# Kernel tuning notes

Measured on AMD Instinct MI355X. Metric: run time of the kernel, lower is better.

Reference implementation:

```python
import jax, jax.numpy as jnp
from jax import lax
import numpy as np

# ---- static configuration (RPN inference path) ----
B = 8
IMG_H, IMG_W = 800, 1216
LEVEL_GRIDS = [(200, 304), (100, 152), (50, 76), (25, 38), (13, 19)]
STRIDES = [4, 8, 16, 32, 64]
SIZES = [32, 64, 128, 256, 512]
RATIOS = np.array([0.5, 1.0, 2.0])
NUM_PER_LEVEL = [h * w * 3 for (h, w) in LEVEL_GRIDS]  # [182400,45600,11400,2850,741]
A_TOTAL = sum(NUM_PER_LEVEL)                            # 242991
PRE_N = 1000   # pre_nms_top_n['testing'], applied per level
POST_N = 1000  # post_nms_top_n['testing']
NMS_THRESH = 0.7
SCORE_THRESH = 0.0
MIN_SIZE = 0.001
BBOX_XFORM_CLIP = float(np.log(1000.0 / 16.0))
LEVEL_OFFSET = 4096.0  # > max image coord, for batched_nms level separation

K_PER_LEVEL = [min(PRE_N, n) for n in NUM_PER_LEVEL]
K_TOTAL = sum(K_PER_LEVEL)  # 4741
LEVELS = jnp.concatenate([jnp.full((k,), i, dtype=jnp.int32)
                          for i, k in enumerate(K_PER_LEVEL)])


def _make_anchors():
    """torchvision-style grid anchors, one scale + 3 aspect ratios per level."""
    all_anchors = []
    for (fh, fw), stride, size in zip(LEVEL_GRIDS, STRIDES, SIZES):
        h_ratios = np.sqrt(RATIOS)
        w_ratios = 1.0 / h_ratios
        ws = w_ratios * size
        hs = h_ratios * size
        base = np.stack([-ws / 2, -hs / 2, ws / 2, hs / 2], axis=1)  # [3,4]
        sx = np.arange(fw, dtype=np.float32) * stride
        sy = np.arange(fh, dtype=np.float32) * stride
        yy, xx = np.meshgrid(sy, sx, indexing='ij')
        shifts = np.stack([xx, yy, xx, yy], axis=-1).reshape(-1, 1, 4)  # [fh*fw,1,4]
        anchors = (shifts + base[None]).reshape(-1, 4)                  # [fh*fw*3,4]
        all_anchors.append(anchors.astype(np.float32))
    return np.concatenate(all_anchors, axis=0)  # [A_TOTAL,4]


def setup_inputs() -> dict:
    key = jax.random.key(0)
    k1, k2 = jax.random.split(key)
    objectness = jax.random.normal(k1, (B, A_TOTAL), dtype=jnp.float32)
    pred_bbox_deltas = jax.random.normal(k2, (B, A_TOTAL, 4), dtype=jnp.float32) * 0.5
    anchors = jnp.asarray(_make_anchors())
    return {"objectness": objectness, "pred_bbox_deltas": pred_bbox_deltas,
            "anchors": anchors}


def _decode(deltas, anchors):
    """BoxCoder.decode with weights (1,1,1,1). deltas [B,A,4], anchors [A,4]."""
    wa = anchors[:, 2] - anchors[:, 0]
    ha = anchors[:, 3] - anchors[:, 1]
    cxa = anchors[:, 0] + 0.5 * wa
    cya = anchors[:, 1] + 0.5 * ha
    dx, dy, dw, dh = deltas[..., 0], deltas[..., 1], deltas[..., 2], deltas[..., 3]
    dw = jnp.minimum(dw, BBOX_XFORM_CLIP)
    dh = jnp.minimum(dh, BBOX_XFORM_CLIP)
    cx = dx * wa + cxa
    cy = dy * ha + cya
    w = jnp.exp(dw) * wa
    h = jnp.exp(dh) * ha
    return jnp.stack([cx - 0.5 * w, cy - 0.5 * h, cx + 0.5 * w, cy + 0.5 * h], axis=-1)


def _per_level_topk(objectness):
    """_get_top_n_idx: per-level top-k with global offsets. Returns [B,K_TOTAL] int32."""
    idxs, offset = [], 0
    for n, k in zip(NUM_PER_LEVEL, K_PER_LEVEL):
        _, ti = lax.top_k(objectness[:, offset:offset + n], k)
        idxs.append(ti + offset)
        offset += n
    return jnp.concatenate(idxs, axis=1)


def _iou(boxes):  # boxes [K,4] -> [K,K]
    area = (boxes[:, 2] - boxes[:, 0]) * (boxes[:, 3] - boxes[:, 1])
    lt = jnp.maximum(boxes[:, None, :2], boxes[None, :, :2])
    rb = jnp.minimum(boxes[:, None, 2:], boxes[None, :, 2:])
    wh = jnp.clip(rb - lt, 0.0)
    inter = wh[..., 0] * wh[..., 1]
    return inter / (area[:, None] + area[None, :] - inter)


def _nms_image(boxes, scores, levels, valid):
    """clip->filter->batched_nms->post_nms_top_n for one image (fixed shapes)."""
    K = boxes.shape[0]
    order = jnp.argsort(-jnp.where(valid, scores, -jnp.inf))
    b = boxes[order]
    s = scores[order]
    v = valid[order]
    lv = levels[order]
    # batched NMS: offset boxes by level so cross-level boxes never overlap
    bb = b + lv.astype(b.dtype)[:, None] * LEVEL_OFFSET
    iou = lax.stop_gradient(_iou(bb))  # keep decisions are non-differentiable
    idxr = jnp.arange(K)

    def body(i, keep):
        sup = (iou[i] > NMS_THRESH) & (idxr > i) & keep[i]
        return keep & ~sup

    keep = lax.fori_loop(0, K, body, v)
    sel = jnp.where(keep, s, -1.0)  # sigmoid scores are > 0
    top_s, top_i = lax.top_k(sel, POST_N)
    kept = top_s > 0.0
    out_b = jnp.where(kept[:, None], b[top_i], 0.0)
    out_s = jnp.where(kept, top_s, 0.0)
    return out_b, out_s


def reference(objectness, pred_bbox_deltas, anchors):
    # box decode for all anchors
    proposals = _decode(pred_bbox_deltas, anchors)          # [B,A,4]
    # per-level topk + gather
    idx = _per_level_topk(objectness)                       # [B,K]
    obj = jnp.take_along_axis(objectness, idx, axis=1)      # [B,K]
    props = jnp.take_along_axis(proposals, idx[..., None], axis=1)  # [B,K,4]
    scores = jax.nn.sigmoid(obj)
    lv = jnp.broadcast_to(LEVELS, idx.shape)
    # clip_boxes_to_image
    x1 = jnp.clip(props[..., 0], 0.0, IMG_W)
    y1 = jnp.clip(props[..., 1], 0.0, IMG_H)
    x2 = jnp.clip(props[..., 2], 0.0, IMG_W)
    y2 = jnp.clip(props[..., 3], 0.0, IMG_H)
    props = jnp.stack([x1, y1, x2, y2], axis=-1)
    # remove_small_boxes + score_thresh
    valid = (x2 - x1 >= MIN_SIZE) & (y2 - y1 >= MIN_SIZE) & (scores >= SCORE_THRESH)
    boxes_out, scores_out = jax.vmap(_nms_image)(props, scores, lv, valid)
    return boxes_out, scores_out  # [B,POST_N,4], [B,POST_N] (zero-padded)
```

## Files before the change

### kernel.cpp

```cpp
#include <hip/hip_runtime.h>
#include <stdint.h>

#pragma clang fp contract(off)

typedef unsigned int u32;
typedef unsigned long long u64;

#define A_TOTAL 242991
#define KTOT    4741

__constant__ int c_LN[5]   = {182400, 45600, 11400, 2850, 741};
__constant__ int c_LOFF[5] = {0, 182400, 228000, 239400, 242250};
__constant__ int c_LK[5]   = {1000, 1000, 1000, 1000, 741};

__constant__ int c_SL[33] = {0,0,0,0,0,0,0,0,0,0,0,0,0,0,0,0,0,0,0,0,0,0,0,
                             1,1,1,1,1,1, 2,2, 3, 4};
__constant__ int c_SS[33] = {0,8192,16384,24576,32768,40960,49152,57344,65536,
                             73728,81920,90112,98304,106496,114688,122880,131072,
                             139264,147456,155648,163840,172032,180224,
                             0,8192,16384,24576,32768,40960, 0,8192, 0, 0};

__constant__ int c_MW[40] = {0,1,2,3, 4,4, 5,5, 6,6, 7,7, 8,8,8, 9,9,9,
                             10,10,10, 11,11,11, 12,12,12,12, 13,13,13,13,
                             14,14,14,14, 15,15,15,15};
__constant__ int c_MR[40] = {0,0,0,0, 0,1, 0,1, 0,1, 0,1, 0,1,2, 0,1,2,
                             0,1,2, 0,1,2, 0,1,2,3, 0,1,2,3,
                             0,1,2,3, 0,1,2,3};

static const size_t OFF_KEEPW    = 0;
static const size_t OFF_HIST     = 0;
static const size_t OFF_SELCNT   = 327680;
static const size_t OFF_CANDCNT  = 327840;
static const size_t OFF_TBIN     = 328000;
static const size_t OFF_CLESS    = 328160;
static const size_t OFF_SELG     = 328320;
static const size_t OFF_CANDG    = 656000;
static const size_t OFF_BOX      = 2270144;
static const size_t OFF_SCORE    = 2876992;
static const size_t OFF_VALID    = 3028704;
static const size_t OFF_MASK     = 3180416;
static const size_t OFF_OUTK     = 8423296;

__device__ __forceinline__ u32 fmap(float f){
  u32 b = __float_as_uint(f);
  return (b & 0x80000000u) ? ~b : (b | 0x80000000u);
}
__device__ __forceinline__ float funmap(u32 m){
  return __uint_as_float((m & 0x80000000u) ? (m & 0x7FFFFFFFu) : ~m);
}

#define ZWS  82000
#define ZOUT 40000
__global__ void __launch_bounds__(256)
k_zero(u32* __restrict__ ws0, u32* __restrict__ outw)
{
  int i = blockIdx.x * 256 + (int)threadIdx.x;
  if (i < ZWS) ws0[i] = 0u;
  else {
    int j = i - ZWS;
    if (j < ZOUT) outw[j] = 0u;
  }
}

__global__ void __launch_bounds__(1024)
k_hist(const float* __restrict__ obj, u32* __restrict__ hist)
{
  int b = blockIdx.x / 33, s = blockIdx.x % 33;
  int l = c_SL[s], start = c_SS[s];
  int cnt = c_LN[l] - start; if (cnt > 8192) cnt = 8192;
  int bl = b * 5 + l;
  __shared__ u32 h[4][2048];
  for (int i = threadIdx.x; i < 8192; i += 1024) ((u32*)h)[i] = 0;
  __syncthreads();
  u32* hw = h[(threadIdx.x >> 6) & 3];
  const float* p = obj + (size_t)b * A_TOTAL + c_LOFF[l] + start;
  int head = (4 - (int)(((size_t)p >> 2) & 3)) & 3;
  if (head > cnt) head = cnt;
  if ((int)threadIdx.x < head) atomicAdd(&hw[(~fmap(p[threadIdx.x])) >> 21], 1u);
  int nvec = (cnt - head) >> 2;
  const float4* pv = (const float4*)(p + head);
  for (int i = threadIdx.x; i < nvec; i += 1024){
    float4 v = pv[i];
    atomicAdd(&hw[(~fmap(v.x)) >> 21], 1u);
    atomicAdd(&hw[(~fmap(v.y)) >> 21], 1u);
    atomicAdd(&hw[(~fmap(v.z)) >> 21], 1u);
    atomicAdd(&hw[(~fmap(v.w)) >> 21], 1u);
  }
  int tail0 = head + (nvec << 2);
  int ntail = cnt - tail0;
  if ((int)threadIdx.x < ntail) atomicAdd(&hw[(~fmap(p[tail0 + threadIdx.x])) >> 21], 1u);
  __syncthreads();
  for (int i = threadIdx.x; i < 2048; i += 1024){
    u32 v = h[0][i] + h[1][i] + h[2][i] + h[3][i];
    if (v) atomicAdd(&hist[bl * 2048 + i], v);
  }
}

__global__ void __launch_bounds__(256)
k_cutoff(u32* __restrict__ hist, u32* __restrict__ tbin, u32* __restrict__ cless)
{
  int bl = blockIdx.x; int l = bl % 5;
  int K = c_LK[l], n = c_LN[l];
  int tid = threadIdx.x;
  __shared__ u32 cum[2048];
  __shared__ u32 part[256];
  __shared__ int s_t;
  u32 vals[8]; u32 sum = 0;
  for (int q = 0; q < 8; ++q){ vals[q] = hist[bl * 2048 + tid * 8 + q]; sum += vals[q]; }
  part[tid] = sum;
  __syncthreads();
  for (int off = 1; off < 256; off <<= 1){
    u32 add = (tid >= off) ? part[tid - off] : 0u;
    __syncthreads();
    part[tid] += add;
    __syncthreads();
  }
  u32 run = (tid > 0) ? part[tid - 1] : 0u;
  for (int q = 0; q < 8; ++q){ run += vals[q]; cum[tid * 8 + q] = run; }
  __syncthreads();
  if (K >= n){ if (tid == 0){ tbin[bl] = 2048u; cless[bl] = (u32)n; } return; }
  if (tid == 0) s_t = 0;
  __syncthreads();
  for (int q = 0; q < 8; ++q){
    int i = tid * 8 + q;
    u32 c = cum[i], cp = (i > 0) ? cum[i - 1] : 0u;
    if (c >= (u32)K && cp < (u32)K) s_t = i;
  }
  __syncthreads();
  if (tid == 0){
    int t = s_t;
    tbin[bl] = (u32)t;
    cless[bl] = (t > 0) ? cum[t - 1] : 0u;
  }
}

#define SELCAP 2048
#define CANDCAP 1024
__global__ void __launch_bounds__(1024)
k_collect(const float* __restrict__ obj, const u32* __restrict__ tbin,
          u32* __restrict__ selcnt, u32* __restrict__ candcnt,
          u64* __restrict__ selg, u64* __restrict__ candg)
{
  int b = blockIdx.x / 33, s = blockIdx.x % 33;
  int l = c_SL[s], start = c_SS[s];
  int cnt = c_LN[l] - start; if (cnt > 8192) cnt = 8192;
  int bl = b * 5 + l;
  u32 t = tbin[bl];
  __shared__ u64 lsel[SELCAP];
  __shared__ u64 lcand[CANDCAP];
  __shared__ u32 lcs, lcc, gbs, gbc;
  if (threadIdx.x == 0){ lcs = 0u; lcc = 0u; }
  __syncthreads();
  const float* p = obj + (size_t)b * A_TOTAL + c_LOFF[l] + start;

  auto push = [&](u32 m, int idx){
    u32 bin = m >> 21;
    u64 key = ((u64)m << 32) | (u32)idx;
    if (bin < t){
      u32 pos = atomicAdd(&lcs, 1u);
      if (pos < SELCAP) lsel[pos] = key;
      else { u32 gp = atomicAdd(&selcnt[bl], 1u); selg[(size_t)bl * 1024 + gp] = key; }
    } else if (bin == t){
      u32 pos = atomicAdd(&lcc, 1u);
      if (pos < CANDCAP) lcand[pos] = key;
      else { u32 gp = atomicAdd(&candcnt[bl], 1u); if (gp < 4096u) candg[(size_t)bl * 4096 + gp] = key; }
    }
  };

  int head = (4 - (int)(((size_t)p >> 2) & 3)) & 3;
  if (head > cnt) head = cnt;
  if ((int)threadIdx.x < head) push(~fmap(p[threadIdx.x]), start + (int)threadIdx.x);
  int nvec = (cnt - head) >> 2;
  const float4* pv = (const float4*)(p + head);
  for (int i = threadIdx.x; i < nvec; i += 1024){
    float4 v = pv[i];
    int e = start + head + (i << 2);
    push(~fmap(v.x), e);
    push(~fmap(v.y), e + 1);
    push(~fmap(v.z), e + 2);
    push(~fmap(v.w), e + 3);
  }
  int tail0 = head + (nvec << 2);
  int ntail = cnt - tail0;
  if ((int)threadIdx.x < ntail) push(~fmap(p[tail0 + threadIdx.x]), start + tail0 + (int)threadIdx.x);
  __syncthreads();
  u32 ns = lcs;  if (ns > SELCAP) ns = SELCAP;
  u32 ncd = lcc; if (ncd > CANDCAP) ncd = CANDCAP;
  if (threadIdx.x == 0){
    gbs = ns  ? atomicAdd(&selcnt[bl],  ns)  : 0u;
    gbc = ncd ? atomicAdd(&candcnt[bl], ncd) : 0u;
  }
  __syncthreads();
  u32 bs = gbs, bc = gbc;
  for (u32 i = threadIdx.x; i < ns; i += 1024)
    selg[(size_t)bl * 1024 + bs + i] = lsel[i];
  for (u32 i = threadIdx.x; i < ncd; i += 1024){
    u32 gp = bc + i;
    if (gp < 4096u) candg[(size_t)bl * 4096 + gp] = lcand[i];
  }
}

__global__ void __launch_bounds__(1024)
k_selectdec(const u32* __restrict__ selcnt, const u32* __restrict__ candcnt,
            const u64* __restrict__ selg, const u64* __restrict__ candg,
            const float* __restrict__ deltas, const float* __restrict__ anchors,
            float* __restrict__ boxes, float* __restrict__ scores, u32* __restrict__ valid)
{
  int bl = blockIdx.x; int b = bl / 5, l = bl % 5;
  int K = c_LK[l];
  int tid = threadIdx.x;
  __shared__ __align__(16) u64 selU[1024];
  __shared__ __align__(16) u64 candU[4098];
  __shared__ u64 keysL[1000];
  u32 ns = selcnt[bl]; if (ns > 1024u) ns = 1024u;
  u32 nc = candcnt[bl]; if (nc > 4096u) nc = 4096u;
  int R = K - (int)ns;
  selU[tid] = (tid < (int)ns) ? selg[(size_t)bl * 1024 + tid] : ~0ULL;
  for (u32 i = tid; i < nc; i += 1024) candU[i] = candg[(size_t)bl * 4096 + i];
  u32 nce = (nc + 1u) & ~1u;
  if (tid == 0 && nce > nc) candU[nc] = ~0ULL;
  __syncthreads();
  if (tid < (int)ns){
    u64 key = selU[tid];
    u32 r = 0;
    #pragma unroll 8
    for (u32 j = 0; j < 1024; j += 2){
      ulonglong2 v = *reinterpret_cast<const ulonglong2*>(&selU[j]);
      r += (v.x < key) + (v.y < key);
    }
    keysL[r] = key;
  }
  if (R > 0){
    for (u32 s = tid; s < nc; s += 1024){
      u64 key = candU[s];
      u32 r = 0;
      #pragma unroll 8
      for (u32 j = 0; j < nce; j += 2){
        ulonglong2 v = *reinterpret_cast<const ulonglong2*>(&candU[j]);
        r += (v.x < key) + (v.y < key);
      }
      if (r < (u32)R) keysL[ns + r] = key;
    }
  }
  __syncthreads();
  if (tid < K){
    u64 key = keysL[tid];
    int g = b * KTOT + l * 1000 + tid;
    u32 idx = (u32)key;
    float o = funmap(~(u32)(key >> 32));
    int ai = c_LOFF[l] + (int)idx;
    const float* a = anchors + (size_t)ai * 4;
    const float* d = deltas + ((size_t)b * A_TOTAL + ai) * 4;
    float a0 = a[0], a1 = a[1], a2 = a[2], a3 = a[3];
    float wa = __fsub_rn(a2, a0), ha = __fsub_rn(a3, a1);
    float cxa = __fadd_rn(a0, __fmul_rn(0.5f, wa));
    float cya = __fadd_rn(a1, __fmul_rn(0.5f, ha));
    float dx = d[0], dy = d[1];
    float dw = fminf(d[2], 4.135166556742356f);
    float dh = fminf(d[3], 4.135166556742356f);
    float cx = __fadd_rn(__fmul_rn(dx, wa), cxa);
    float cy = __fadd_rn(__fmul_rn(dy, ha), cya);
    float w  = __fmul_rn(expf(dw), wa);
    float h  = __fmul_rn(expf(dh), ha);
    float hw = __fmul_rn(0.5f, w), hh = __fmul_rn(0.5f, h);
    float x1 = __fsub_rn(cx, hw), y1 = __fsub_rn(cy, hh);
    float x2 = __fadd_rn(cx, hw), y2 = __fadd_rn(cy, hh);
    x1 = fminf(fmaxf(x1, 0.0f), 1216.0f);
    x2 = fminf(fmaxf(x2, 0.0f), 1216.0f);
    y1 = fminf(fmaxf(y1, 0.0f), 800.0f);
    y2 = fminf(fmaxf(y2, 0.0f), 800.0f);
    float s = __fdiv_rn(1.0f, __fadd_rn(1.0f, expf(-o)));
    int v = (__fsub_rn(x2, x1) >= 0.001f) && (__fsub_rn(y2, y1) >= 0.001f) && (s >= 0.0f);
    float* bo = boxes + (size_t)g * 4;
    bo[0] = x1; bo[1] = y1; bo[2] = x2; bo[3] = y2;
    scores[g] = s;
    valid[g] = (u32)v;
  }
}

__global__ void __launch_bounds__(256)
k_mask(const float* __restrict__ boxes, u64* __restrict__ mask)
{
  int b = blockIdx.x / 184, s = blockIdx.x % 184;
  int l, idx;
  if (s < 160){ l = s / 40; idx = s % 40; }
  else        { l = 4;      idx = s - 160; }
  int w = c_MW[idx], rb = c_MR[idx];
  int N = c_LK[l];
  int koff = l * 1000;
  float offv = (float)(l * 4096);
  __shared__ float sjx1[64], sjy1[64], sjx2[64], sjy2[64], sjar[64];
  int jbase = w * 64;
  if (threadIdx.x < 64){
    int j = jbase + (int)threadIdx.x;
    float x1, y1, x2, y2, ar;
    if (j < N){
      float4 p = ((const float4*)boxes)[(size_t)(b * KTOT + koff + j)];
      x1 = __fadd_rn(p.x, offv); y1 = __fadd_rn(p.y, offv);
      x2 = __fadd_rn(p.z, offv); y2 = __fadd_rn(p.w, offv);
      ar = __fmul_rn(__fsub_rn(x2, x1), __fsub_rn(y2, y1));
    } else {
      x1 = 3e38f; y1 = 3e38f; x2 = -3e38f; y2 = -3e38f; ar = 0.f;
    }
    sjx1[threadIdx.x] = x1; sjy1[threadIdx.x] = y1;
    sjx2[threadIdx.x] = x2; sjy2[threadIdx.x] = y2; sjar[threadIdx.x] = ar;
  }
  __syncthreads();
  int i = rb * 256 + (int)threadIdx.x;
  int rows = (w + 1) * 64; if (rows > N) rows = N;
  if (i >= rows) return;
  float4 p = ((const float4*)boxes)[(size_t)(b * KTOT + koff + i)];
  float bx1 = __fadd_rn(p.x, offv), by1 = __fadd_rn(p.y, offv);
  float bx2 = __fadd_rn(p.z, offv), by2 = __fadd_rn(p.w, offv);
  float bar = __fmul_rn(__fsub_rn(bx2, bx1), __fsub_rn(by2, by1));
  u64 bw = 0;
  #pragma unroll 16
  for (int jj = 0; jj < 64; ++jj){
    int j = jbase + jj;
    float ltx = fmaxf(bx1, sjx1[jj]), lty = fmaxf(by1, sjy1[jj]);
    float rbx = fminf(bx2, sjx2[jj]), rby = fminf(by2, sjy2[jj]);
    float wx = fmaxf(__fsub_rn(rbx, ltx), 0.0f);
    float wy = fmaxf(__fsub_rn(rby, lty), 0.0f);
    float inter = __fmul_rn(wx, wy);
    bool sup = false;
    if (inter > 0.0f && j > i){
      float den = __fsub_rn(__fadd_rn(bar, sjar[jj]), inter);
      sup = __fdiv_rn(inter, den) > 0.7f;
    }
    bw |= ((u64)sup) << jj;
  }
  mask[((size_t)(b * 5 + l) * 16 + w) * 1024 + i] = bw;
}

__global__ void __launch_bounds__(256)
k_nms(const u64* __restrict__ mask, const u32* __restrict__ valid,
      const float* __restrict__ scores, u64* __restrict__ outk,
      u64* __restrict__ keepw)
{
  int bl = blockIdx.x; int b = bl / 5, l = bl % 5;
  int N = c_LK[l], koff = l * 1000;
  int WN = (N + 63) >> 6;
  int tid = threadIdx.x;
  __shared__ u64 s_kw[16];
  __shared__ u64 s_m[7680];
  const u64* mb = mask + (size_t)bl * 16 * 1024;
  int wstage = (WN < 15) ? WN : 15;
  for (int w = 0; w < wstage; ++w){
    int rows = (w + 1) * 64;
    int base = 32 * w * (w + 1);
    for (int r = tid; r < rows; r += 256)
      s_m[base + r] = mb[(size_t)w * 1024 + r];
  }
  __syncthreads();
  if (tid < 64){
    int lane = tid;
    for (int c = 0; c < WN; ++c){
      int i = c * 64 + lane;
      int pred = (i < N) && (valid[(size_t)b * KTOT + koff + i] != 0u);
      u64 bal = __ballot(pred);
      if (lane == 0) s_kw[c] = bal;
    }
    for (int w = 0; w < WN; ++w){
      u64 kwv = s_kw[w];
      u64 supl = 0;
      if (w < 15){
        int base = 32 * w * (w + 1);
        for (int jb = 0; jb < w; ++jb){
          u64 kb = s_kw[jb];
          u64 m = s_m[base + jb * 64 + lane];
          supl |= (((kb >> lane) & 1ULL) ? m : 0ULL);
        }
      } else {
        for (int jb = 0; jb < w; ++jb){
          u64 kb = s_kw[jb];
          u64 m = mb[(size_t)w * 1024 + jb * 64 + lane];
          supl |= (((kb >> lane) & 1ULL) ? m : 0ULL);
        }
      }
      int jr = w * 64 + lane;
      u64 rowl;
      if (w < 15) rowl = s_m[32 * w * (w + 1) + jr];
      else        rowl = (jr < N) ? mb[(size_t)w * 1024 + jr] : 0ULL;
      bool inC = ((kwv >> lane) & 1ULL) != 0ULL;
      u64 rkw = rowl & kwv;
      u64 confl = inC ? rkw : 0ULL;
      u32 a0 = (u32)supl, a1 = (u32)(supl >> 32);
      u32 a2 = (u32)confl, a3 = (u32)(confl >> 32);
      for (int off = 32; off; off >>= 1){
        a0 |= __shfl_xor(a0, off);
        a1 |= __shfl_xor(a1, off);
        a2 |= __shfl_xor(a2, off);
        a3 |= __shfl_xor(a3, off);
      }
      supl = ((u64)a1 << 32) | a0;
      u64 conf = ((u64)a3 << 32) | a2;
      u64 srcb = __ballot(inC && (rkw != 0ULL));
      u64 cur = kwv & ~supl;
      u64 kept = cur;
      if (((srcb & cur) != 0ULL) && ((conf & cur) != 0ULL)){
        u32 rowl_lo = (u32)rowl, rowl_hi = (u32)(rowl >> 32);
        u64 act = cur & (srcb | conf);
        while (act){
          int ib  = __ffsll((unsigned long long)act) - 1;
          int ibs = __builtin_amdgcn_readfirstlane(ib);
          u64 bit = 1ULL << ibs;
          act &= ~bit;
          if (kept & bit){
            u32 rlo = (u32)__builtin_amdgcn_readlane((int)rowl_lo, ibs);
            u32 rhi = (u32)__builtin_amdgcn_readlane((int)rowl_hi, ibs);
            u64 r   = ((u64)rhi << 32) | rlo;
            kept &= ~r;
            act  &= ~r;
          }
        }
      }
      if (lane == 0) s_kw[w] = kept;
    }
  }
  __syncthreads();
  if (tid < 16) keepw[(size_t)bl * 16 + tid] = (tid < WN) ? s_kw[tid] : 0ULL;
  for (int i = tid; i < N; i += 256){
    u64 key = ~0ULL;
    if ((s_kw[i >> 6] >> (i & 63)) & 1ULL){
      float sc = scores[(size_t)b * KTOT + koff + i];
      key = ((u64)(~fmap(sc)) << 32) | (u32)(koff + i);
    }
    outk[(size_t)b * KTOT + koff + i] = key;
  }
}

#define CMPN 1024
__global__ void __launch_bounds__(256)
k_rank(const u64* __restrict__ outk, const u64* __restrict__ keepw,
       const float* __restrict__ boxes, float* __restrict__ out)
{
  int b = blockIdx.x / 19, chunk = blockIdx.x % 19;
  int tid = threadIdx.x;
  __shared__ u64 cmp[5 * CMPN];
  __shared__ u64 kw[80];
  for (int i = tid; i < 5 * CMPN; i += 256) cmp[i] = ~0ULL;
  if (tid < 80) kw[tid] = keepw[(size_t)b * 80 + tid];
  __syncthreads();
  for (int i = tid; i < KTOT; i += 256){
    u64 key = outk[(size_t)b * KTOT + i];
    if (key != ~0ULL){
      int l = i / 1000; if (l > 4) l = 4;
      int li = i - l * 1000;
      int wi = li >> 6, bit = li & 63;
      const u64* kwl = &kw[l * 16];
      int r = __popcll(kwl[wi] & ((1ULL << bit) - 1ULL));
      for (int w = 0; w < wi; ++w) r += __popcll(kwl[w]);
      cmp[l * CMPN + r] = key;
    }
  }
  __syncthreads();
  int i = chunk * 256 + tid;
  if (i >= KTOT) return;
  u64 key = outk[(size_t)b * KTOT + i];
  if (key == ~0ULL) return;
  int l = i / 1000; if (l > 4) l = 4;
  int li = i - l * 1000;
  int wi = li >> 6, bit = li & 63;
  const u64* kwl = &kw[l * 16];
  int rank = __popcll(kwl[wi] & ((1ULL << bit) - 1ULL));
  for (int w = 0; w < wi; ++w) rank += __popcll(kwl[w]);
  #pragma unroll
  for (int lo = 0; lo < 5; ++lo){
    if (lo == l) continue;
    int pos = 0;
    #pragma unroll
    for (int s = 512; s > 0; s >>= 1)
      if (cmp[lo * CMPN + pos + s - 1] < key) pos += s;
    rank += pos;
  }
  if (rank < 1000){
    float4 bx = ((const float4*)boxes)[(size_t)(b * KTOT + i)];
    ((float4*)out)[(size_t)(b * 1000 + rank)] = bx;
    out[32000 + b * 1000 + rank] = funmap(~(u32)(key >> 32));
  }
}

extern "C" void kernel_launch(void* const* d_in, const int* in_sizes, int n_in,
                              void* d_out, int out_size, void* d_ws, size_t ws_size,
                              hipStream_t stream)
{
  (void)in_sizes; (void)n_in; (void)out_size; (void)ws_size;
  const float* obj     = (const float*)d_in[0];
  const float* deltas  = (const float*)d_in[1];
  const float* anchors = (const float*)d_in[2];
  float* out = (float*)d_out;
  char* ws = (char*)d_ws;

  u32* hist    = (u32*)(ws + OFF_HIST);
  u64* keepw   = (u64*)(ws + OFF_KEEPW);
  u32* selcnt  = (u32*)(ws + OFF_SELCNT);
  u32* candcnt = (u32*)(ws + OFF_CANDCNT);
  u32* tbin    = (u32*)(ws + OFF_TBIN);
  u32* cless   = (u32*)(ws + OFF_CLESS);
  u64* selg    = (u64*)(ws + OFF_SELG);
  u64* candg   = (u64*)(ws + OFF_CANDG);
  float* boxes = (float*)(ws + OFF_BOX);
  float* score = (float*)(ws + OFF_SCORE);
  u32* valid   = (u32*)(ws + OFF_VALID);
  u64* mask    = (u64*)(ws + OFF_MASK);
  u64* outk    = (u64*)(ws + OFF_OUTK);

  hipLaunchKernelGGL(k_zero,      dim3((ZWS + ZOUT + 255) / 256), dim3(256), 0, stream,
                     (u32*)ws, (u32*)out);
  hipLaunchKernelGGL(k_hist,      dim3(264),  dim3(1024), 0, stream, obj, hist);
  hipLaunchKernelGGL(k_cutoff,    dim3(40),   dim3(256),  0, stream, hist, tbin, cless);
  hipLaunchKernelGGL(k_collect,   dim3(264),  dim3(1024), 0, stream, obj, tbin, selcnt, candcnt, selg, candg);
  hipLaunchKernelGGL(k_selectdec, dim3(40),   dim3(1024), 0, stream, selcnt, candcnt, selg, candg,
                     deltas, anchors, boxes, score, valid);
  hipLaunchKernelGGL(k_mask,      dim3(1472), dim3(256),  0, stream, boxes, mask);
  hipLaunchKernelGGL(k_nms,       dim3(40),   dim3(256),  0, stream, mask, valid, score, outk, keepw);
  hipLaunchKernelGGL(k_rank,      dim3(152),  dim3(256),  0, stream, outk, keepw, boxes, out);
}
```

Before: 126.6 us.

## Fuse histogram cutoff search into collect kernel and move output zeroing into NMS

```diff
diff --git a/kernel.cpp b/kernel.cpp
--- a/kernel.cpp
+++ b/kernel.cpp
@@ -31,8 +31,6 @@
 static const size_t OFF_HIST     = 0;
 static const size_t OFF_SELCNT   = 327680;
 static const size_t OFF_CANDCNT  = 327840;
-static const size_t OFF_TBIN     = 328000;
-static const size_t OFF_CLESS    = 328160;
 static const size_t OFF_SELG     = 328320;
 static const size_t OFF_CANDG    = 656000;
 static const size_t OFF_BOX      = 2270144;
@@ -49,17 +47,12 @@
   return __uint_as_float((m & 0x80000000u) ? (m & 0x7FFFFFFFu) : ~m);
 }
 
-#define ZWS  82000
-#define ZOUT 40000
+#define ZWS 82000
 __global__ void __launch_bounds__(256)
-k_zero(u32* __restrict__ ws0, u32* __restrict__ outw)
+k_zero(u32* __restrict__ ws0)
 {
   int i = blockIdx.x * 256 + (int)threadIdx.x;
   if (i < ZWS) ws0[i] = 0u;
-  else {
-    int j = i - ZWS;
-    if (j < ZOUT) outw[j] = 0u;
-  }
 }
 
 __global__ void __launch_bounds__(1024)
@@ -96,48 +89,10 @@
   }
 }
 
-__global__ void __launch_bounds__(256)
-k_cutoff(u32* __restrict__ hist, u32* __restrict__ tbin, u32* __restrict__ cless)
-{
-  int bl = blockIdx.x; int l = bl % 5;
-  int K = c_LK[l], n = c_LN[l];
-  int tid = threadIdx.x;
-  __shared__ u32 cum[2048];
-  __shared__ u32 part[256];
-  __shared__ int s_t;
-  u32 vals[8]; u32 sum = 0;
-  for (int q = 0; q < 8; ++q){ vals[q] = hist[bl * 2048 + tid * 8 + q]; sum += vals[q]; }
-  part[tid] = sum;
-  __syncthreads();
-  for (int off = 1; off < 256; off <<= 1){
-    u32 add = (tid >= off) ? part[tid - off] : 0u;
-    __syncthreads();
-    part[tid] += add;
-    __syncthreads();
-  }
-  u32 run = (tid > 0) ? part[tid - 1] : 0u;
-  for (int q = 0; q < 8; ++q){ run += vals[q]; cum[tid * 8 + q] = run; }
-  __syncthreads();
-  if (K >= n){ if (tid == 0){ tbin[bl] = 2048u; cless[bl] = (u32)n; } return; }
-  if (tid == 0) s_t = 0;
-  __syncthreads();
-  for (int q = 0; q < 8; ++q){
-    int i = tid * 8 + q;
-    u32 c = cum[i], cp = (i > 0) ? cum[i - 1] : 0u;
-    if (c >= (u32)K && cp < (u32)K) s_t = i;
-  }
-  __syncthreads();
-  if (tid == 0){
-    int t = s_t;
-    tbin[bl] = (u32)t;
-    cless[bl] = (t > 0) ? cum[t - 1] : 0u;
-  }
-}
-
 #define SELCAP 2048
 #define CANDCAP 1024
 __global__ void __launch_bounds__(1024)
-k_collect(const float* __restrict__ obj, const u32* __restrict__ tbin,
+k_collect(const float* __restrict__ obj, const u32* __restrict__ hist,
           u32* __restrict__ selcnt, u32* __restrict__ candcnt,
           u64* __restrict__ selg, u64* __restrict__ candg)
 {
@@ -145,12 +100,42 @@
   int l = c_SL[s], start = c_SS[s];
   int cnt = c_LN[l] - start; if (cnt > 8192) cnt = 8192;
   int bl = b * 5 + l;
-  u32 t = tbin[bl];
+  int K = c_LK[l], n = c_LN[l];
+  int tid = threadIdx.x;
   __shared__ u64 lsel[SELCAP];
   __shared__ u64 lcand[CANDCAP];
-  __shared__ u32 lcs, lcc, gbs, gbc;
-  if (threadIdx.x == 0){ lcs = 0u; lcc = 0u; }
-  __syncthreads();
+  __shared__ u32 part[1024];
+  __shared__ u32 lcs, lcc, gbs, gbc, s_tval;
+  if (tid == 0){ lcs = 0u; lcc = 0u; }
+  if (K < n) part[tid] = hist[bl * 2048 + 2 * tid] + hist[bl * 2048 + 2 * tid + 1];
+  __syncthreads();
+  if (K < n && tid < 64){
+    u32 gs = 0;
+    #pragma unroll
+    for (int q = 0; q < 16; ++q) gs += part[tid * 16 + q];
+    u32 c = gs;
+    for (int off = 1; off < 64; off <<= 1){
+      u32 u = __shfl_up(c, off);
+      if (tid >= off) c += u;
+    }
+    u32 cp = c - gs;
+    bool crossing = (c >= (u32)K) && (cp < (u32)K);
+    u64 bal = __ballot(crossing);
+    int jj = __ffsll((unsigned long long)bal) - 1;
+    u32 cpj = (u32)__shfl((int)cp, jj);
+    u32 bv = (tid < 32) ? hist[bl * 2048 + jj * 32 + tid] : 0u;
+    u32 cb = bv;
+    for (int off2 = 1; off2 < 32; off2 <<= 1){
+      u32 u2 = __shfl_up(cb, off2);
+      if ((int)(tid & 31) >= off2) cb += u2;
+    }
+    bool cross2 = (tid < 32) && (cpj + cb >= (u32)K) && (cpj + cb - bv < (u32)K);
+    u64 bal2 = __ballot(cross2);
+    int kk = __ffsll((unsigned long long)bal2) - 1;
+    if (tid == 0) s_tval = (u32)(jj * 32 + kk);
+  }
+  __syncthreads();
+  u32 t = (K >= n) ? 2048u : s_tval;
   const float* p = obj + (size_t)b * A_TOTAL + c_LOFF[l] + start;
 
   auto push = [&](u32 m, int idx){
@@ -169,10 +154,10 @@
 
   int head = (4 - (int)(((size_t)p >> 2) & 3)) & 3;
   if (head > cnt) head = cnt;
-  if ((int)threadIdx.x < head) push(~fmap(p[threadIdx.x]), start + (int)threadIdx.x);
+  if (tid < head) push(~fmap(p[tid]), start + tid);
   int nvec = (cnt - head) >> 2;
   const float4* pv = (const float4*)(p + head);
-  for (int i = threadIdx.x; i < nvec; i += 1024){
+  for (int i = tid; i < nvec; i += 1024){
     float4 v = pv[i];
     int e = start + head + (i << 2);
     push(~fmap(v.x), e);
@@ -182,19 +167,19 @@
   }
   int tail0 = head + (nvec << 2);
   int ntail = cnt - tail0;
-  if ((int)threadIdx.x < ntail) push(~fmap(p[tail0 + threadIdx.x]), start + tail0 + (int)threadIdx.x);
+  if (tid < ntail) push(~fmap(p[tail0 + tid]), start + tail0 + tid);
   __syncthreads();
   u32 ns = lcs;  if (ns > SELCAP) ns = SELCAP;
   u32 ncd = lcc; if (ncd > CANDCAP) ncd = CANDCAP;
-  if (threadIdx.x == 0){
+  if (tid == 0){
     gbs = ns  ? atomicAdd(&selcnt[bl],  ns)  : 0u;
     gbc = ncd ? atomicAdd(&candcnt[bl], ncd) : 0u;
   }
   __syncthreads();
   u32 bs = gbs, bc = gbc;
-  for (u32 i = threadIdx.x; i < ns; i += 1024)
+  for (u32 i = tid; i < ns; i += 1024)
     selg[(size_t)bl * 1024 + bs + i] = lsel[i];
-  for (u32 i = threadIdx.x; i < ncd; i += 1024){
+  for (u32 i = tid; i < ncd; i += 1024){
     u32 gp = bc + i;
     if (gp < 4096u) candg[(size_t)bl * 4096 + gp] = lcand[i];
   }
@@ -335,12 +320,13 @@
 __global__ void __launch_bounds__(256)
 k_nms(const u64* __restrict__ mask, const u32* __restrict__ valid,
       const float* __restrict__ scores, u64* __restrict__ outk,
-      u64* __restrict__ keepw)
+      u64* __restrict__ keepw, float* __restrict__ outz)
 {
   int bl = blockIdx.x; int b = bl / 5, l = bl % 5;
   int N = c_LK[l], koff = l * 1000;
   int WN = (N + 63) >> 6;
   int tid = threadIdx.x;
+  for (int i = tid; i < 1000; i += 256) outz[bl * 1000 + i] = 0.0f;
   __shared__ u64 s_kw[16];
   __shared__ u64 s_m[7680];
   const u64* mb = mask + (size_t)bl * 16 * 1024;
@@ -495,8 +481,6 @@
   u64* keepw   = (u64*)(ws + OFF_KEEPW);
   u32* selcnt  = (u32*)(ws + OFF_SELCNT);
   u32* candcnt = (u32*)(ws + OFF_CANDCNT);
-  u32* tbin    = (u32*)(ws + OFF_TBIN);
-  u32* cless   = (u32*)(ws + OFF_CLESS);
   u64* selg    = (u64*)(ws + OFF_SELG);
   u64* candg   = (u64*)(ws + OFF_CANDG);
   float* boxes = (float*)(ws + OFF_BOX);
@@ -505,14 +489,12 @@
   u64* mask    = (u64*)(ws + OFF_MASK);
   u64* outk    = (u64*)(ws + OFF_OUTK);
 
-  hipLaunchKernelGGL(k_zero,      dim3((ZWS + ZOUT + 255) / 256), dim3(256), 0, stream,
-                     (u32*)ws, (u32*)out);
+  hipLaunchKernelGGL(k_zero,      dim3((ZWS + 255) / 256), dim3(256), 0, stream, (u32*)ws);
   hipLaunchKernelGGL(k_hist,      dim3(264),  dim3(1024), 0, stream, obj, hist);
-  hipLaunchKernelGGL(k_cutoff,    dim3(40),   dim3(256),  0, stream, hist, tbin, cless);
-  hipLaunchKernelGGL(k_collect,   dim3(264),  dim3(1024), 0, stream, obj, tbin, selcnt, candcnt, selg, candg);
+  hipLaunchKernelGGL(k_collect,   dim3(264),  dim3(1024), 0, stream, obj, hist, selcnt, candcnt, selg, candg);
   hipLaunchKernelGGL(k_selectdec, dim3(40),   dim3(1024), 0, stream, selcnt, candcnt, selg, candg,
                      deltas, anchors, boxes, score, valid);
   hipLaunchKernelGGL(k_mask,      dim3(1472), dim3(256),  0, stream, boxes, mask);
-  hipLaunchKernelGGL(k_nms,       dim3(40),   dim3(256),  0, stream, mask, valid, score, outk, keepw);
+  hipLaunchKernelGGL(k_nms,       dim3(40),   dim3(256),  0, stream, mask, valid, score, outk, keepw, out);
   hipLaunchKernelGGL(k_rank,      dim3(152),  dim3(256),  0, stream, outk, keepw, boxes, out);
 }
```

After: 125.0 us, median of 2. About the same (-1.3%).
